# Performance work log

Measured on AMD Instinct MI355X. Metric: run time of the kernel, lower is better.

Reference implementation:

```python
import jax, jax.numpy as jnp
import numpy as np

N = 100000
E = 1600000
K = 3
DIMS = [64, 64, 64, 32, 16]


def setup_inputs() -> dict:
    key = jax.random.key(0)
    ks = jax.random.split(key, 12)
    inp = {
        "x": jax.random.normal(ks[0], (N, DIMS[0]), jnp.float32),
        "edge_index": jax.random.randint(ks[1], (2, E), 0, N, dtype=jnp.int64),
        "edge_weight": jax.random.uniform(ks[2], (E,), jnp.float32),
    }
    for i in range(4):
        scale = 1.0 / np.sqrt(DIMS[i] * K).astype(np.float32)
        inp[f"W{i+1}"] = jax.random.normal(ks[3 + 2 * i], (K, DIMS[i], DIMS[i + 1]), jnp.float32) * scale
        inp[f"b{i+1}"] = jnp.zeros((DIMS[i + 1],), jnp.float32)
    return inp


def _cheb_norm(edge_index, edge_weight, n):
    # PyG ChebConv norm with normalization='sym', lambda_max=2:
    # L = I - D^{-1/2} A D^{-1/2}; L_hat = 2L/lambda_max - I = -D^{-1/2} A D^{-1/2} (zero diag)
    row, col = edge_index[0], edge_index[1]
    w = jnp.where(row == col, 0.0, edge_weight)  # remove self loops
    deg = jax.ops.segment_sum(w, row, num_segments=n)
    dinv = jnp.where(deg > 0, jax.lax.rsqrt(deg), 0.0)  # inf -> 0 masking
    return -dinv[row] * w * dinv[col]


def _cheb_conv(x, edge_index, norm, W, b):
    row, col = edge_index[0], edge_index[1]
    n = x.shape[0]

    def prop(t):  # sparse L_hat @ t via gather + segment scatter-add
        return jax.ops.segment_sum(norm[:, None] * t[row], col, num_segments=n)

    Tx0 = x
    out = Tx0 @ W[0]
    Tx1 = prop(Tx0)
    out = out + Tx1 @ W[1]
    for k in range(2, W.shape[0]):
        Tx2 = 2.0 * prop(Tx1) - Tx0  # Chebyshev recurrence
        out = out + Tx2 @ W[k]
        Tx0, Tx1 = Tx1, Tx2
    return out + b


def reference(x, edge_index, edge_weight, W1, b1, W2, b2, W3, b3, W4, b4):
    norm = _cheb_norm(edge_index, edge_weight, x.shape[0])
    h = x
    for W, b in ((W1, b1), (W2, b2), (W3, b3), (W4, b4)):
        h = jax.nn.sigmoid(_cheb_conv(h, edge_index, norm, W, b))
    return h
```

## Files before the change

kernel.cpp:

```cpp
#include <hip/hip_runtime.h>
#include <math.h>


typedef __attribute__((ext_vector_type(8))) short short8_t;
typedef __attribute__((ext_vector_type(4))) short short4_t;
typedef __attribute__((ext_vector_type(4))) float f32x4;

#define NPP 512
#define FSH 9
#define CHUNK 2048
#define NXCD 8

__device__ __forceinline__ float bf2f(short s) {
    return __int_as_float(((int)(unsigned short)s) << 16);
}
__device__ __forceinline__ short f2bf(float f) {
    unsigned u = __float_as_uint(f);
    return (short)((u + 0x7FFFu + ((u >> 16) & 1u)) >> 16);
}

__device__ __forceinline__ int chunk_of_block(int bid, int B) {
    int xcd = bid & (NXCD - 1);
    int i = bid >> 3;
    int q = B >> 3, r = B & (NXCD - 1);
    return (xcd < r) ? xcd * (q + 1) + i : r * (q + 1) + (xcd - r) * q + i;
}

__device__ __forceinline__ int epk_row(unsigned u) { return (int)(u & 0x1FFFFu); }
__device__ __forceinline__ float epk_val(unsigned u) {
    return __uint_as_float((u >> 17) << 17);
}


__global__ __launch_bounds__(256) void f2b_kernel(
        const float* __restrict__ in, short* __restrict__ out, long m) {
    long i = ((long)blockIdx.x * 256 + threadIdx.x) * 4;
    if (i >= m) return;
    float4 v = *reinterpret_cast<const float4*>(in + i);
    short4_t s;
    s[0] = f2bf(v.x); s[1] = f2bf(v.y); s[2] = f2bf(v.z); s[3] = f2bf(v.w);
    *reinterpret_cast<short4_t*>(out + i) = s;
}


__global__ __launch_bounds__(256) void prep_kernel(
        const float* __restrict__ W1, const float* __restrict__ W2,
        const float* __restrict__ W3, const float* __restrict__ W4,
        short8_t* __restrict__ wpk1, short8_t* __restrict__ wpk2,
        short8_t* __restrict__ wpkm, short8_t* __restrict__ wpk4) {
    int idx = blockIdx.x * 256 + threadIdx.x;
    if (idx >= 4032) return;
    short8_t out;
    if (idx < 3072) {
        const float* W = (idx < 1536) ? W1 : W2;
        int f = (idx < 1536) ? idx : idx - 1536;
        int lane = f & 63, ct = (f >> 6) & 3, s = f >> 8;
        int li = lane & 15, lg = lane >> 4;
        int p = s >> 1;
        int col = ct * 16 + li;
#pragma unroll
        for (int e = 0; e < 8; ++e) {
            int k = (s & 1) * 32 + lg * 8 + e;
            int base = k * 64 + col;
            float v = (p == 0) ? W[base] - W[8192 + base]
                    : (p == 1) ? W[4096 + base]
                               : 2.0f * W[8192 + base];
            out[e] = f2bf(v);
        }
        ((idx < 1536) ? wpk1 : wpk2)[f] = out;
    } else if (idx < 3840) {
        int f = idx - 3072;
        int lane = f & 63, q = f >> 6;
        int s = q / 6, ct = q % 6;
        int li = lane & 15, lg = lane >> 4;
        int g = ct >> 1;
        int cl = (ct & 1) * 16 + li;
#pragma unroll
        for (int e = 0; e < 8; ++e) {
            int k = s * 32 + lg * 8 + e;
            int base = k * 32 + cl;
            float v = (g == 0) ? W3[base] - W3[4096 + base]
                    : (g == 1) ? W3[2048 + base]
                               : W3[4096 + base];
            out[e] = f2bf(v);
        }
        wpkm[f] = out;
    } else {
        int f = idx - 3840;
        int lane = f & 63, s = f >> 6;
        int li = lane & 15, lg = lane >> 4;
#pragma unroll
        for (int e = 0; e < 8; ++e) {
            int k = lg * 8 + e;
            int base = k * 16 + li;
            float v = (s == 0) ? W4[base] - W4[1024 + base]
                    : (s == 1) ? W4[512 + base]
                               : 2.0f * W4[1024 + base];
            out[e] = f2bf(v);
        }
        wpk4[f] = out;
    }
}


__global__ __launch_bounds__(256) void count_kernel(
        const int* __restrict__ row, const int* __restrict__ col,
        int* __restrict__ cntC, int* __restrict__ cntR, int P, int E) {
    __shared__ int hc[2][256], hr[2][256];
    for (int i = threadIdx.x; i < P; i += 256) {
        hc[0][i] = 0; hc[1][i] = 0; hr[0][i] = 0; hr[1][i] = 0;
    }
    __syncthreads();
    int chunk = chunk_of_block(blockIdx.x, gridDim.x);
    int cp = threadIdx.x & 1;
    int base = chunk * CHUNK;
    int lim = min(E, base + CHUNK);
    for (int e = base + threadIdx.x; e < lim; e += 256) {
        atomicAdd(&hc[cp][col[e] >> FSH], 1);
        atomicAdd(&hr[cp][row[e] >> FSH], 1);
    }
    __syncthreads();
    long o = (long)chunk * P;
    for (int i = threadIdx.x; i < P; i += 256) {
        cntC[o + i] = hc[0][i] + hc[1][i];
        cntR[o + i] = hr[0][i] + hr[1][i];
    }
}

__global__ __launch_bounds__(256) void colscan_kernel(
        int* __restrict__ cntC, int* __restrict__ cntR,
        int* __restrict__ ptotC, int* __restrict__ ptotR, int P, int B) {
    int bid = blockIdx.x;
    int* m; int* ptot; int p;
    if (bid < P) { m = cntC; ptot = ptotC; p = bid; }
    else         { m = cntR; ptot = ptotR; p = bid - P; }
    __shared__ int sh[256];
    int run = 0;
    for (int b0 = 0; b0 < B; b0 += 256) {
        int b = b0 + threadIdx.x;
        int v = (b < B) ? m[(long)b * P + p] : 0;
        sh[threadIdx.x] = v;
        __syncthreads();
        for (int o = 1; o < 256; o <<= 1) {
            int t = (threadIdx.x >= o) ? sh[threadIdx.x - o] : 0;
            __syncthreads();
            sh[threadIdx.x] += t;
            __syncthreads();
        }
        if (b < B) m[(long)b * P + p] = run + sh[threadIdx.x] - v;
        run += sh[255];
        __syncthreads();
    }
    if (threadIdx.x == 0) ptot[p] = run;
}

__global__ __launch_bounds__(256) void pscan_kernel(
        const int* __restrict__ ptotC, const int* __restrict__ ptotR,
        int* __restrict__ pofsC, int* __restrict__ pofsR,
        int* __restrict__ ofs, int P, int n, int E) {
    __shared__ int sh[256];
    int tid = threadIdx.x;
    int v = (tid < P) ? ptotC[tid] : 0;
    sh[tid] = v;
    __syncthreads();
    for (int o = 1; o < 256; o <<= 1) {
        int t = (tid >= o) ? sh[tid - o] : 0;
        __syncthreads();
        sh[tid] += t;
        __syncthreads();
    }
    if (tid < P) pofsC[tid] = sh[tid] - v;
    if (tid == 0) pofsC[P] = E;
    __syncthreads();
    v = (tid < P) ? ptotR[tid] : 0;
    sh[tid] = v;
    __syncthreads();
    for (int o = 1; o < 256; o <<= 1) {
        int t = (tid >= o) ? sh[tid - o] : 0;
        __syncthreads();
        sh[tid] += t;
        __syncthreads();
    }
    if (tid < P) pofsR[tid] = sh[tid] - v;
    if (tid == 0) { pofsR[P] = E; ofs[n] = E; }
}

__global__ __launch_bounds__(256) void scatter_kernel(
        const int* __restrict__ row, const int* __restrict__ col,
        const float* __restrict__ ew,
        const int* __restrict__ cntC, const int* __restrict__ cntR,
        const int* __restrict__ pofsC, const int* __restrict__ pofsR,
        int2* __restrict__ bufC, unsigned* __restrict__ bufR, int P, int E) {
    __shared__ int hc[256], hr[256];
    int chunk = chunk_of_block(blockIdx.x, gridDim.x);
    long o = (long)chunk * P;
    for (int i = threadIdx.x; i < P; i += 256) {
        hc[i] = pofsC[i] + cntC[o + i];
        hr[i] = pofsR[i] + cntR[o + i];
    }
    __syncthreads();
    int base = chunk * CHUNK;
    int lim = min(E, base + CHUNK);
    for (int e = base + threadIdx.x; e < lim; e += 256) {
        int r = row[e], c = col[e];
        float w = (r == c) ? 0.0f : ew[e];
        unsigned wb = __float_as_uint(w);
        int pc = atomicAdd(&hc[c >> FSH], 1);
        bufC[pc] = make_int2((int)(((unsigned)(c & (NPP - 1)) << 23) | (unsigned)r), (int)wb);
        int pr = atomicAdd(&hr[r >> FSH], 1);
        bufR[pr] = ((unsigned)(r & (NPP - 1)) << 23) | (wb >> 9);
    }
}

__global__ __launch_bounds__(512) void dinv_kernel(
        const unsigned* __restrict__ bufR, const int* __restrict__ rofs,
        float* __restrict__ dinv, int n) {
    int p = blockIdx.x;
    __shared__ float s[NPP];
    s[threadIdx.x] = 0.0f;
    __syncthreads();
    int beg = rofs[p], end = rofs[p + 1];
    for (int k = beg + threadIdx.x; k < end; k += 512) {
        unsigned u = bufR[k];
        atomicAdd(&s[u >> 23], __uint_as_float((u & 0x7FFFFFu) << 9));
    }
    __syncthreads();
    int node = (p << FSH) + threadIdx.x;
    if (node < n) {
        float d = s[threadIdx.x];
        dinv[node] = d > 0.0f ? rsqrtf(d) : 0.0f;
    }
}

__global__ __launch_bounds__(512) void fine_csr_kernel(
        const int2* __restrict__ bufC, const int* __restrict__ pofs,
        const float* __restrict__ dinv, int* __restrict__ ofs,
        unsigned* __restrict__ epk, int n) {
    int p = blockIdx.x;
    int tid = threadIdx.x;
    __shared__ int hist[NPP];
    __shared__ int sc[NPP];
    __shared__ float dc[NPP];
    hist[tid] = 0;
    int node = (p << FSH) + tid;
    dc[tid] = (node < n) ? dinv[node] : 0.0f;
    __syncthreads();
    int beg = pofs[p], end = pofs[p + 1];
    for (int k = beg + tid; k < end; k += 512)
        atomicAdd(&hist[((unsigned)bufC[k].x) >> 23], 1);
    __syncthreads();
    int v = hist[tid];
    sc[tid] = v;
    __syncthreads();
    for (int o = 1; o < 512; o <<= 1) {
        int t = (tid >= o) ? sc[tid - o] : 0;
        __syncthreads();
        sc[tid] += t;
        __syncthreads();
    }
    int mybase = beg + sc[tid] - v;
    if (node < n) ofs[node] = mybase;
    hist[tid] = mybase;
    __syncthreads();
    for (int k = beg + tid; k < end; k += 512) {
        int2 ed = bufC[k];
        unsigned key = (unsigned)ed.x;
        int fc = key >> 23;
        int r = (int)(key & 0x7FFFFFu);
        float w = __int_as_float(ed.y);
        float nrm = -dinv[r] * w * dc[fc];
        unsigned nb = __float_as_uint(nrm);
        unsigned n15 = (nb + 0xFFFFu + ((nb >> 17) & 1u)) >> 17;
        int pos = atomicAdd(&hist[fc], 1);
        epk[pos] = (n15 << 17) | (unsigned)r;
    }
}


template <int D>
__global__ __launch_bounds__(256) void agg_kernel(
        const int* __restrict__ ofs, const unsigned* __restrict__ epk,
        const short* __restrict__ tb, short* __restrict__ outb, int n) {
    constexpr int LPN = D / 8;
    int idx = blockIdx.x * 256 + threadIdx.x;
    int node = idx / LPN;
    int l = idx % LPN;
    if (node >= n) return;
    int beg = ofs[node], end = ofs[node + 1];
    float a[8] = {0.f, 0.f, 0.f, 0.f, 0.f, 0.f, 0.f, 0.f};
    const short* tc = tb + l * 8;
    int k = beg;
    for (; k + 8 <= end; k += 8) {
        unsigned ev[8];
        short8_t xv[8];
#pragma unroll
        for (int u = 0; u < 8; ++u) ev[u] = epk[k + u];
#pragma unroll
        for (int u = 0; u < 8; ++u)
            xv[u] = *reinterpret_cast<const short8_t*>(tc + (long)epk_row(ev[u]) * D);
#pragma unroll
        for (int u = 0; u < 8; ++u) {
            float v = epk_val(ev[u]);
#pragma unroll
            for (int j = 0; j < 8; ++j) a[j] = fmaf(v, bf2f(xv[u][j]), a[j]);
        }
    }
    for (; k + 4 <= end; k += 4) {
        unsigned ev[4];
        short8_t xv[4];
#pragma unroll
        for (int u = 0; u < 4; ++u) ev[u] = epk[k + u];
#pragma unroll
        for (int u = 0; u < 4; ++u)
            xv[u] = *reinterpret_cast<const short8_t*>(tc + (long)epk_row(ev[u]) * D);
#pragma unroll
        for (int u = 0; u < 4; ++u) {
            float v = epk_val(ev[u]);
#pragma unroll
            for (int j = 0; j < 8; ++j) a[j] = fmaf(v, bf2f(xv[u][j]), a[j]);
        }
    }
    for (; k < end; ++k) {
        unsigned e0 = epk[k];
        short8_t x0 = *reinterpret_cast<const short8_t*>(tc + (long)epk_row(e0) * D);
        float v = epk_val(e0);
#pragma unroll
        for (int j = 0; j < 8; ++j) a[j] = fmaf(v, bf2f(x0[j]), a[j]);
    }
    short8_t s;
#pragma unroll
    for (int j = 0; j < 8; ++j) s[j] = f2bf(a[j]);
    *reinterpret_cast<short8_t*>(outb + (long)node * D + l * 8) = s;
}


__global__ __launch_bounds__(256) void agg_dual_kernel(
        const int* __restrict__ ofs, const unsigned* __restrict__ epk,
        const short* __restrict__ tb, short* __restrict__ Q1b,
        short* __restrict__ Q2b, int n) {
    int idx = blockIdx.x * 256 + threadIdx.x;
    int node = idx >> 3;
    int l = idx & 7;
    if (node >= n) return;
    int beg = ofs[node], end = ofs[node + 1];
    float a[8] = {0.f, 0.f, 0.f, 0.f, 0.f, 0.f, 0.f, 0.f};
    const short* tc = tb + l * 8;
    int k = beg;
    for (; k + 8 <= end; k += 8) {
        unsigned ev[8];
        short8_t xv[8];
#pragma unroll
        for (int u = 0; u < 8; ++u) ev[u] = epk[k + u];
#pragma unroll
        for (int u = 0; u < 8; ++u)
            xv[u] = *reinterpret_cast<const short8_t*>(tc + (long)epk_row(ev[u]) * 64);
#pragma unroll
        for (int u = 0; u < 8; ++u) {
            float v = epk_val(ev[u]);
#pragma unroll
            for (int j = 0; j < 8; ++j) a[j] = fmaf(v, bf2f(xv[u][j]), a[j]);
        }
    }
    for (; k + 4 <= end; k += 4) {
        unsigned ev[4];
        short8_t xv[4];
#pragma unroll
        for (int u = 0; u < 4; ++u) ev[u] = epk[k + u];
#pragma unroll
        for (int u = 0; u < 4; ++u)
            xv[u] = *reinterpret_cast<const short8_t*>(tc + (long)epk_row(ev[u]) * 64);
#pragma unroll
        for (int u = 0; u < 4; ++u) {
            float v = epk_val(ev[u]);
#pragma unroll
            for (int j = 0; j < 8; ++j) a[j] = fmaf(v, bf2f(xv[u][j]), a[j]);
        }
    }
    for (; k < end; ++k) {
        unsigned e0 = epk[k];
        short8_t x0 = *reinterpret_cast<const short8_t*>(tc + (long)epk_row(e0) * 64);
        float v = epk_val(e0);
#pragma unroll
        for (int j = 0; j < 8; ++j) a[j] = fmaf(v, bf2f(x0[j]), a[j]);
    }
    short* ob = (l < 4) ? Q1b : Q2b;
    long o = (long)node * 32 + (l & 3) * 8;
    short8_t s;
#pragma unroll
    for (int j = 0; j < 8; ++j) s[j] = f2bf(a[j]);
    *reinterpret_cast<short8_t*>(ob + o) = s;
}


__global__ __launch_bounds__(256) void agg_fin_kernel(
        const int* __restrict__ ofs, const unsigned* __restrict__ epk,
        const short* __restrict__ Q2b, const float* __restrict__ S,
        const short* __restrict__ Q1b, short* __restrict__ outb, int n) {
    int idx = blockIdx.x * 256 + threadIdx.x;
    int node = idx >> 2;
    int l = idx & 3;
    if (node >= n) return;
    int beg = ofs[node], end = ofs[node + 1];
    float a[8] = {0.f, 0.f, 0.f, 0.f, 0.f, 0.f, 0.f, 0.f};
    const short* tc = Q2b + l * 8;
    int k = beg;
    for (; k + 4 <= end; k += 4) {
        unsigned ev[4];
        short8_t xv[4];
#pragma unroll
        for (int u = 0; u < 4; ++u) ev[u] = epk[k + u];
#pragma unroll
        for (int u = 0; u < 4; ++u)
            xv[u] = *reinterpret_cast<const short8_t*>(tc + (long)epk_row(ev[u]) * 32);
#pragma unroll
        for (int u = 0; u < 4; ++u) {
            float v = epk_val(ev[u]);
#pragma unroll
            for (int j = 0; j < 8; ++j) a[j] = fmaf(v, bf2f(xv[u][j]), a[j]);
        }
    }
    for (; k < end; ++k) {
        unsigned e0 = epk[k];
        short8_t x0 = *reinterpret_cast<const short8_t*>(tc + (long)epk_row(e0) * 32);
        float v = epk_val(e0);
#pragma unroll
        for (int j = 0; j < 8; ++j) a[j] = fmaf(v, bf2f(x0[j]), a[j]);
    }
    long o = (long)node * 32 + l * 8;
    float4 s0 = *reinterpret_cast<const float4*>(S + o);
    float4 s1 = *reinterpret_cast<const float4*>(S + o + 4);
    short8_t q1 = *reinterpret_cast<const short8_t*>(Q1b + o);
    float sv[8] = {s0.x, s0.y, s0.z, s0.w, s1.x, s1.y, s1.z, s1.w};
    short8_t r;
#pragma unroll
    for (int j = 0; j < 8; ++j) {
        float z = sv[j] + bf2f(q1[j]) + 2.0f * a[j];
        r[j] = f2bf(1.0f / (1.0f + expf(-z)));
    }
    *reinterpret_cast<short8_t*>(outb + o) = r;
}


__global__ __launch_bounds__(256) void gemm3_mfma(
        const short* __restrict__ t0b, const short* __restrict__ t1b,
        const short* __restrict__ t2b, const short8_t* __restrict__ wpk,
        const float* __restrict__ b, short* __restrict__ outb, int n) {
    const int tid = threadIdx.x;
    const int wave = tid >> 6;
    const int lane = tid & 63;
    const int li = lane & 15;
    const int lg = lane >> 4;

    short8_t bfr[6][4];
#pragma unroll
    for (int s = 0; s < 6; ++s)
#pragma unroll
        for (int ct = 0; ct < 4; ++ct)
            bfr[s][ct] = wpk[(s * 4 + ct) * 64 + lane];

    float bias_v[4];
#pragma unroll
    for (int ct = 0; ct < 4; ++ct) bias_v[ct] = b[ct * 16 + li];

#pragma unroll
    for (int t = 0; t < 2; ++t) {
        int r0 = blockIdx.x * 128 + wave * 32 + t * 16;
        if (r0 >= n) continue;
        int rA = r0 + li;
        if (rA >= n) rA = n - 1;
        f32x4 acc[4] = {{0.f, 0.f, 0.f, 0.f}, {0.f, 0.f, 0.f, 0.f},
                        {0.f, 0.f, 0.f, 0.f}, {0.f, 0.f, 0.f, 0.f}};
#pragma unroll
        for (int s = 0; s < 6; ++s) {
            const short* src = (s < 2) ? t0b : (s < 4) ? t1b : t2b;
            int k = (s & 1) * 32 + lg * 8;
            short8_t a = *reinterpret_cast<const short8_t*>(src + (long)rA * 64 + k);
#pragma unroll
            for (int ct = 0; ct < 4; ++ct)
                acc[ct] = __builtin_amdgcn_mfma_f32_16x16x32_bf16(a, bfr[s][ct], acc[ct], 0, 0, 0);
        }
#pragma unroll
        for (int ct = 0; ct < 4; ++ct) {
#pragma unroll
            for (int reg = 0; reg < 4; ++reg) {
                int row = r0 + lg * 4 + reg;
                if (row < n) {
                    float z = acc[ct][reg] + bias_v[ct];
                    float res = 1.0f / (1.0f + expf(-z));
                    outb[(long)row * 64 + ct * 16 + li] = f2bf(res);
                }
            }
        }
    }
}

__global__ __launch_bounds__(256) void gemm_multi_mfma(
        const short* __restrict__ hb, const short8_t* __restrict__ wpk,
        const float* __restrict__ b, short* __restrict__ P12b,
        float* __restrict__ S, int n) {
    const int tid = threadIdx.x;
    const int wave = tid >> 6;
    const int lane = tid & 63;
    const int li = lane & 15;
    const int lg = lane >> 4;

    short8_t bfr[2][6];
#pragma unroll
    for (int s = 0; s < 2; ++s)
#pragma unroll
        for (int ct = 0; ct < 6; ++ct)
            bfr[s][ct] = wpk[(s * 6 + ct) * 64 + lane];

    float bS0 = b[li], bS1 = b[16 + li];

#pragma unroll
    for (int t = 0; t < 2; ++t) {
        int r0 = blockIdx.x * 128 + wave * 32 + t * 16;
        if (r0 >= n) continue;
        int rA = r0 + li;
        if (rA >= n) rA = n - 1;
        f32x4 acc[6] = {{0.f, 0.f, 0.f, 0.f}, {0.f, 0.f, 0.f, 0.f},
                        {0.f, 0.f, 0.f, 0.f}, {0.f, 0.f, 0.f, 0.f},
                        {0.f, 0.f, 0.f, 0.f}, {0.f, 0.f, 0.f, 0.f}};
#pragma unroll
        for (int s = 0; s < 2; ++s) {
            int k = s * 32 + lg * 8;
            short8_t a = *reinterpret_cast<const short8_t*>(hb + (long)rA * 64 + k);
#pragma unroll
            for (int ct = 0; ct < 6; ++ct)
                acc[ct] = __builtin_amdgcn_mfma_f32_16x16x32_bf16(a, bfr[s][ct], acc[ct], 0, 0, 0);
        }
#pragma unroll
        for (int ct = 0; ct < 6; ++ct) {
            int g = ct >> 1;
            int cl = (ct & 1) * 16 + li;
#pragma unroll
            for (int reg = 0; reg < 4; ++reg) {
                int row = r0 + lg * 4 + reg;
                if (row >= n) continue;
                float v = acc[ct][reg];
                if (g == 0) {
                    S[(long)row * 32 + cl] = v + ((ct & 1) ? bS1 : bS0);
                } else if (g == 1) {
                    P12b[(long)row * 64 + cl] = f2bf(v);
                } else {
                    P12b[(long)row * 64 + 32 + cl] = f2bf(v);
                }
            }
        }
    }
}

__global__ __launch_bounds__(256) void gemm4_mfma(
        const short* __restrict__ t0b, const short* __restrict__ t1b,
        const short* __restrict__ t2b, const short8_t* __restrict__ wpk,
        const float* __restrict__ b, float* __restrict__ out, int n) {
    const int tid = threadIdx.x;
    const int wave = tid >> 6;
    const int lane = tid & 63;
    const int li = lane & 15;
    const int lg = lane >> 4;

    short8_t bfr[3];
#pragma unroll
    for (int s = 0; s < 3; ++s) bfr[s] = wpk[s * 64 + lane];

    float bias_v = b[li];

#pragma unroll
    for (int t = 0; t < 2; ++t) {
        int r0 = blockIdx.x * 128 + wave * 32 + t * 16;
        if (r0 >= n) continue;
        int rA = r0 + li;
        if (rA >= n) rA = n - 1;
        f32x4 acc = {0.f, 0.f, 0.f, 0.f};
        int k = lg * 8;
        short8_t a0 = *reinterpret_cast<const short8_t*>(t0b + (long)rA * 32 + k);
        acc = __builtin_amdgcn_mfma_f32_16x16x32_bf16(a0, bfr[0], acc, 0, 0, 0);
        short8_t a1 = *reinterpret_cast<const short8_t*>(t1b + (long)rA * 32 + k);
        acc = __builtin_amdgcn_mfma_f32_16x16x32_bf16(a1, bfr[1], acc, 0, 0, 0);
        short8_t a2 = *reinterpret_cast<const short8_t*>(t2b + (long)rA * 32 + k);
        acc = __builtin_amdgcn_mfma_f32_16x16x32_bf16(a2, bfr[2], acc, 0, 0, 0);
#pragma unroll
        for (int reg = 0; reg < 4; ++reg) {
            int row = r0 + lg * 4 + reg;
            if (row < n) {
                float z = acc[reg] + bias_v;
                out[(long)row * 16 + li] = 1.0f / (1.0f + expf(-z));
            }
        }
    }
}


static inline int ceil_div_l(long a, long b) { return (int)((a + b - 1) / b); }

extern "C" void kernel_launch(void* const* d_in, const int* in_sizes, int n_in,
                              void* d_out, int out_size, void* d_ws, size_t ws_size,
                              hipStream_t stream) {
    const float* x  = (const float*)d_in[0];
    const int*   ei = (const int*)d_in[1];
    const float* ew = (const float*)d_in[2];
    const float* W1 = (const float*)d_in[3];  const float* b1 = (const float*)d_in[4];
    const float* W2 = (const float*)d_in[5];  const float* b2 = (const float*)d_in[6];
    const float* W3 = (const float*)d_in[7];  const float* b3 = (const float*)d_in[8];
    const float* W4 = (const float*)d_in[9];  const float* b4 = (const float*)d_in[10];

    const int E = in_sizes[2];
    const int n = in_sizes[0] / 64;
    const int* row = ei;
    const int* col = ei + E;
    const int P = (n + NPP - 1) / NPP;
    const int B = (E + CHUNK - 1) / CHUNK;

    char* ws = (char*)d_ws;
    size_t off = 0;
    auto alloc = [&](size_t bytes) -> void* {
        void* p = ws + off;
        off += (bytes + 255) & ~(size_t)255;
        return p;
    };
    int*      cntC = (int*)alloc((size_t)B * P * sizeof(int));
    int*      cntR = (int*)alloc((size_t)B * P * sizeof(int));
    int*      ptotC = (int*)alloc(256 * sizeof(int));
    int*      ptotR = (int*)alloc(256 * sizeof(int));
    int*      pofsC = (int*)alloc((256 + 1) * sizeof(int));
    int*      pofsR = (int*)alloc((256 + 1) * sizeof(int));
    float*    dinv = (float*)alloc((size_t)n * sizeof(float));
    int*      ofs  = (int*)alloc((size_t)(n + 1) * sizeof(int));
    int2*     bufC = (int2*)alloc((size_t)E * sizeof(int2));
    unsigned* bufR = (unsigned*)alloc((size_t)E * sizeof(unsigned));
    unsigned* epk  = (unsigned*)alloc((size_t)E * sizeof(unsigned));
    short*    hbA  = (short*)alloc((size_t)n * 64 * sizeof(short));
    short*    hbB  = (short*)alloc((size_t)n * 64 * sizeof(short));
    short*    t1b  = (short*)alloc((size_t)n * 64 * sizeof(short));
    short*    Ub   = (short*)alloc((size_t)n * 64 * sizeof(short));
    float*    S    = (float*)alloc((size_t)n * 32 * sizeof(float));
    short8_t* wpk1 = (short8_t*)alloc(1536 * sizeof(short8_t));
    short8_t* wpk2 = (short8_t*)alloc(1536 * sizeof(short8_t));
    short8_t* wpkm = (short8_t*)alloc(768 * sizeof(short8_t));
    short8_t* wpk4 = (short8_t*)alloc(192 * sizeof(short8_t));
    if (off > ws_size) return;

    f2b_kernel<<<ceil_div_l((long)n * 16, 256), 256, 0, stream>>>(x, hbA, (long)n * 64);
    prep_kernel<<<16, 256, 0, stream>>>(W1, W2, W3, W4, wpk1, wpk2, wpkm, wpk4);

    count_kernel<<<B, 256, 0, stream>>>(row, col, cntC, cntR, P, E);
    colscan_kernel<<<2 * P, 256, 0, stream>>>(cntC, cntR, ptotC, ptotR, P, B);
    pscan_kernel<<<1, 256, 0, stream>>>(ptotC, ptotR, pofsC, pofsR, ofs, P, n, E);
    scatter_kernel<<<B, 256, 0, stream>>>(row, col, ew, cntC, cntR, pofsC, pofsR,
                                          bufC, bufR, P, E);
    dinv_kernel<<<P, 512, 0, stream>>>(bufR, pofsR, dinv, n);
    fine_csr_kernel<<<P, 512, 0, stream>>>(bufC, pofsC, dinv, ofs, epk, n);

    const int ab64 = ceil_div_l((long)n * 8, 256);
    const int ab32 = ceil_div_l((long)n * 4, 256);
    const int gb = ceil_div_l(n, 128);

    agg_kernel<64><<<ab64, 256, 0, stream>>>(ofs, epk, hbA, t1b, n);
    agg_kernel<64><<<ab64, 256, 0, stream>>>(ofs, epk, t1b, Ub, n);
    gemm3_mfma<<<gb, 256, 0, stream>>>(hbA, t1b, Ub, wpk1, b1, hbB, n);

    agg_kernel<64><<<ab64, 256, 0, stream>>>(ofs, epk, hbB, t1b, n);
    agg_kernel<64><<<ab64, 256, 0, stream>>>(ofs, epk, t1b, Ub, n);
    gemm3_mfma<<<gb, 256, 0, stream>>>(hbB, t1b, Ub, wpk2, b2, hbA, n);

    {
        short* P12b = t1b;
        short* Q1b  = Ub;
        short* Q2b  = Ub + (size_t)n * 32;
        short* hb3  = hbB;
        gemm_multi_mfma<<<gb, 256, 0, stream>>>(hbA, wpkm, b3, P12b, S, n);
        agg_dual_kernel<<<ab64, 256, 0, stream>>>(ofs, epk, P12b, Q1b, Q2b, n);
        agg_fin_kernel<<<ab32, 256, 0, stream>>>(ofs, epk, Q2b, S, Q1b, hb3, n);
    }

    agg_kernel<32><<<ab32, 256, 0, stream>>>(ofs, epk, hbB, t1b, n);
    agg_kernel<32><<<ab32, 256, 0, stream>>>(ofs, epk, t1b, Ub, n);
    gemm4_mfma<<<gb, 256, 0, stream>>>(hbB, t1b, Ub, wpk4, b4, (float*)d_out, n);
}
```

Baseline: 360.1 us.

## Double CSR partition size to 1024 nodes and fuse input-conversion with weight prep

Result: slower. 376.1 us (+4.5%).

```diff
diff --git a/kernel.cpp b/kernel.cpp
--- a/kernel.cpp
+++ b/kernel.cpp
@@ -6,8 +6,8 @@
 typedef __attribute__((ext_vector_type(4))) short short4_t;
 typedef __attribute__((ext_vector_type(4))) float f32x4;
 
-#define NPP 512
-#define FSH 9
+#define NPP 1024
+#define FSH 10
 #define CHUNK 2048
 #define NXCD 8
 
@@ -32,25 +32,23 @@
 }
 
 
-__global__ __launch_bounds__(256) void f2b_kernel(
-        const float* __restrict__ in, short* __restrict__ out, long m) {
-    long i = ((long)blockIdx.x * 256 + threadIdx.x) * 4;
-    if (i >= m) return;
-    float4 v = *reinterpret_cast<const float4*>(in + i);
-    short4_t s;
-    s[0] = f2bf(v.x); s[1] = f2bf(v.y); s[2] = f2bf(v.z); s[3] = f2bf(v.w);
-    *reinterpret_cast<short4_t*>(out + i) = s;
-}
-
-
-__global__ __launch_bounds__(256) void prep_kernel(
+__global__ __launch_bounds__(256) void init_kernel(
+        const float* __restrict__ in, short* __restrict__ out, long m,
         const float* __restrict__ W1, const float* __restrict__ W2,
         const float* __restrict__ W3, const float* __restrict__ W4,
         short8_t* __restrict__ wpk1, short8_t* __restrict__ wpk2,
         short8_t* __restrict__ wpkm, short8_t* __restrict__ wpk4) {
-    int idx = blockIdx.x * 256 + threadIdx.x;
+    long gi = (long)blockIdx.x * 256 + threadIdx.x;
+    long i4 = gi * 4;
+    if (i4 < m) {
+        float4 v = *reinterpret_cast<const float4*>(in + i4);
+        short4_t s;
+        s[0] = f2bf(v.x); s[1] = f2bf(v.y); s[2] = f2bf(v.z); s[3] = f2bf(v.w);
+        *reinterpret_cast<short4_t*>(out + i4) = s;
+    }
+    int idx = (int)gi;
     if (idx >= 4032) return;
-    short8_t out;
+    short8_t o;
     if (idx < 3072) {
         const float* W = (idx < 1536) ? W1 : W2;
         int f = (idx < 1536) ? idx : idx - 1536;
@@ -65,9 +63,9 @@
             float v = (p == 0) ? W[base] - W[8192 + base]
                     : (p == 1) ? W[4096 + base]
                                : 2.0f * W[8192 + base];
-            out[e] = f2bf(v);
-        }
-        ((idx < 1536) ? wpk1 : wpk2)[f] = out;
+            o[e] = f2bf(v);
+        }
+        ((idx < 1536) ? wpk1 : wpk2)[f] = o;
     } else if (idx < 3840) {
         int f = idx - 3072;
         int lane = f & 63, q = f >> 6;
@@ -82,9 +80,9 @@
             float v = (g == 0) ? W3[base] - W3[4096 + base]
                     : (g == 1) ? W3[2048 + base]
                                : W3[4096 + base];
-            out[e] = f2bf(v);
-        }
-        wpkm[f] = out;
+            o[e] = f2bf(v);
+        }
+        wpkm[f] = o;
     } else {
         int f = idx - 3840;
         int lane = f & 63, s = f >> 6;
@@ -96,9 +94,9 @@
             float v = (s == 0) ? W4[base] - W4[1024 + base]
                     : (s == 1) ? W4[512 + base]
                                : 2.0f * W4[1024 + base];
-            out[e] = f2bf(v);
-        }
-        wpk4[f] = out;
+            o[e] = f2bf(v);
+        }
+        wpk4[f] = o;
     }
 }
 
@@ -106,7 +104,7 @@
 __global__ __launch_bounds__(256) void count_kernel(
         const int* __restrict__ row, const int* __restrict__ col,
         int* __restrict__ cntC, int* __restrict__ cntR, int P, int E) {
-    __shared__ int hc[2][256], hr[2][256];
+    __shared__ int hc[2][128], hr[2][128];
     for (int i = threadIdx.x; i < P; i += 256) {
         hc[0][i] = 0; hc[1][i] = 0; hr[0][i] = 0; hr[1][i] = 0;
     }
@@ -185,13 +183,14 @@
     if (tid == 0) { pofsR[P] = E; ofs[n] = E; }
 }
 
+
 __global__ __launch_bounds__(256) void scatter_kernel(
         const int* __restrict__ row, const int* __restrict__ col,
         const float* __restrict__ ew,
         const int* __restrict__ cntC, const int* __restrict__ cntR,
         const int* __restrict__ pofsC, const int* __restrict__ pofsR,
         int2* __restrict__ bufC, unsigned* __restrict__ bufR, int P, int E) {
-    __shared__ int hc[256], hr[256];
+    __shared__ int hc[128], hr[128];
     int chunk = chunk_of_block(blockIdx.x, gridDim.x);
     long o = (long)chunk * P;
     for (int i = threadIdx.x; i < P; i += 256) {
@@ -206,13 +205,13 @@
         float w = (r == c) ? 0.0f : ew[e];
         unsigned wb = __float_as_uint(w);
         int pc = atomicAdd(&hc[c >> FSH], 1);
-        bufC[pc] = make_int2((int)(((unsigned)(c & (NPP - 1)) << 23) | (unsigned)r), (int)wb);
+        bufC[pc] = make_int2((int)(((unsigned)(c & (NPP - 1)) << 22) | (unsigned)r), (int)wb);
         int pr = atomicAdd(&hr[r >> FSH], 1);
-        bufR[pr] = ((unsigned)(r & (NPP - 1)) << 23) | (wb >> 9);
-    }
-}
-
-__global__ __launch_bounds__(512) void dinv_kernel(
+        bufR[pr] = ((unsigned)(r & (NPP - 1)) << 22) | (wb >> 10);
+    }
+}
+
+__global__ __launch_bounds__(1024) void dinv_kernel(
         const unsigned* __restrict__ bufR, const int* __restrict__ rofs,
         float* __restrict__ dinv, int n) {
     int p = blockIdx.x;
@@ -220,9 +219,9 @@
     s[threadIdx.x] = 0.0f;
     __syncthreads();
     int beg = rofs[p], end = rofs[p + 1];
-    for (int k = beg + threadIdx.x; k < end; k += 512) {
+    for (int k = beg + threadIdx.x; k < end; k += 1024) {
         unsigned u = bufR[k];
-        atomicAdd(&s[u >> 23], __uint_as_float((u & 0x7FFFFFu) << 9));
+        atomicAdd(&s[u >> 22], __uint_as_float((u & 0x3FFFFFu) << 10));
     }
     __syncthreads();
     int node = (p << FSH) + threadIdx.x;
@@ -232,7 +231,7 @@
     }
 }
 
-__global__ __launch_bounds__(512) void fine_csr_kernel(
+__global__ __launch_bounds__(1024) void fine_csr_kernel(
         const int2* __restrict__ bufC, const int* __restrict__ pofs,
         const float* __restrict__ dinv, int* __restrict__ ofs,
         unsigned* __restrict__ epk, int n) {
@@ -246,13 +245,13 @@
     dc[tid] = (node < n) ? dinv[node] : 0.0f;
     __syncthreads();
     int beg = pofs[p], end = pofs[p + 1];
-    for (int k = beg + tid; k < end; k += 512)
-        atomicAdd(&hist[((unsigned)bufC[k].x) >> 23], 1);
+    for (int k = beg + tid; k < end; k += 1024)
+        atomicAdd(&hist[((unsigned)bufC[k].x) >> 22], 1);
     __syncthreads();
     int v = hist[tid];
     sc[tid] = v;
     __syncthreads();
-    for (int o = 1; o < 512; o <<= 1) {
+    for (int o = 1; o < 1024; o <<= 1) {
         int t = (tid >= o) ? sc[tid - o] : 0;
         __syncthreads();
         sc[tid] += t;
@@ -262,11 +261,11 @@
     if (node < n) ofs[node] = mybase;
     hist[tid] = mybase;
     __syncthreads();
-    for (int k = beg + tid; k < end; k += 512) {
+    for (int k = beg + tid; k < end; k += 1024) {
         int2 ed = bufC[k];
         unsigned key = (unsigned)ed.x;
-        int fc = key >> 23;
-        int r = (int)(key & 0x7FFFFFu);
+        int fc = key >> 22;
+        int r = (int)(key & 0x3FFFFFu);
         float w = __int_as_float(ed.y);
         float nrm = -dinv[r] * w * dc[fc];
         unsigned nb = __float_as_uint(nrm);
@@ -622,10 +621,10 @@
     };
     int*      cntC = (int*)alloc((size_t)B * P * sizeof(int));
     int*      cntR = (int*)alloc((size_t)B * P * sizeof(int));
-    int*      ptotC = (int*)alloc(256 * sizeof(int));
-    int*      ptotR = (int*)alloc(256 * sizeof(int));
-    int*      pofsC = (int*)alloc((256 + 1) * sizeof(int));
-    int*      pofsR = (int*)alloc((256 + 1) * sizeof(int));
+    int*      ptotC = (int*)alloc(128 * sizeof(int));
+    int*      ptotR = (int*)alloc(128 * sizeof(int));
+    int*      pofsC = (int*)alloc((128 + 1) * sizeof(int));
+    int*      pofsR = (int*)alloc((128 + 1) * sizeof(int));
     float*    dinv = (float*)alloc((size_t)n * sizeof(float));
     int*      ofs  = (int*)alloc((size_t)(n + 1) * sizeof(int));
     int2*     bufC = (int2*)alloc((size_t)E * sizeof(int2));
@@ -642,16 +641,16 @@
     short8_t* wpk4 = (short8_t*)alloc(192 * sizeof(short8_t));
     if (off > ws_size) return;
 
-    f2b_kernel<<<ceil_div_l((long)n * 16, 256), 256, 0, stream>>>(x, hbA, (long)n * 64);
-    prep_kernel<<<16, 256, 0, stream>>>(W1, W2, W3, W4, wpk1, wpk2, wpkm, wpk4);
+    init_kernel<<<ceil_div_l((long)n * 16, 256), 256, 0, stream>>>(
+        x, hbA, (long)n * 64, W1, W2, W3, W4, wpk1, wpk2, wpkm, wpk4);
 
     count_kernel<<<B, 256, 0, stream>>>(row, col, cntC, cntR, P, E);
     colscan_kernel<<<2 * P, 256, 0, stream>>>(cntC, cntR, ptotC, ptotR, P, B);
     pscan_kernel<<<1, 256, 0, stream>>>(ptotC, ptotR, pofsC, pofsR, ofs, P, n, E);
     scatter_kernel<<<B, 256, 0, stream>>>(row, col, ew, cntC, cntR, pofsC, pofsR,
                                           bufC, bufR, P, E);
-    dinv_kernel<<<P, 512, 0, stream>>>(bufR, pofsR, dinv, n);
-    fine_csr_kernel<<<P, 512, 0, stream>>>(bufC, pofsC, dinv, ofs, epk, n);
+    dinv_kernel<<<P, 1024, 0, stream>>>(bufR, pofsR, dinv, n);
+    fine_csr_kernel<<<P, 1024, 0, stream>>>(bufC, pofsC, dinv, ofs, epk, n);
 
     const int ab64 = ceil_div_l((long)n * 8, 256);
     const int ab32 = ceil_div_l((long)n * 4, 256);
```

## Merge x-to-bf16 and weight packing kernels; double edge chunk size

Applied to the files above, without the earlier changes.

Result: no change. 354.0 us (-1.7%).

```diff
diff --git a/kernel.cpp b/kernel.cpp
--- a/kernel.cpp
+++ b/kernel.cpp
@@ -8,7 +8,7 @@
 
 #define NPP 512
 #define FSH 9
-#define CHUNK 2048
+#define CHUNK 4096
 #define NXCD 8
 
 __device__ __forceinline__ float bf2f(short s) {
@@ -32,25 +32,23 @@
 }
 
 
-__global__ __launch_bounds__(256) void f2b_kernel(
-        const float* __restrict__ in, short* __restrict__ out, long m) {
-    long i = ((long)blockIdx.x * 256 + threadIdx.x) * 4;
-    if (i >= m) return;
-    float4 v = *reinterpret_cast<const float4*>(in + i);
-    short4_t s;
-    s[0] = f2bf(v.x); s[1] = f2bf(v.y); s[2] = f2bf(v.z); s[3] = f2bf(v.w);
-    *reinterpret_cast<short4_t*>(out + i) = s;
-}
-
-
-__global__ __launch_bounds__(256) void prep_kernel(
+__global__ __launch_bounds__(256) void init_kernel(
+        const float* __restrict__ in, short* __restrict__ out, long m,
         const float* __restrict__ W1, const float* __restrict__ W2,
         const float* __restrict__ W3, const float* __restrict__ W4,
         short8_t* __restrict__ wpk1, short8_t* __restrict__ wpk2,
         short8_t* __restrict__ wpkm, short8_t* __restrict__ wpk4) {
-    int idx = blockIdx.x * 256 + threadIdx.x;
+    long gi = (long)blockIdx.x * 256 + threadIdx.x;
+    long i4 = gi * 4;
+    if (i4 < m) {
+        float4 v = *reinterpret_cast<const float4*>(in + i4);
+        short4_t s;
+        s[0] = f2bf(v.x); s[1] = f2bf(v.y); s[2] = f2bf(v.z); s[3] = f2bf(v.w);
+        *reinterpret_cast<short4_t*>(out + i4) = s;
+    }
+    int idx = (int)gi;
     if (idx >= 4032) return;
-    short8_t out;
+    short8_t o;
     if (idx < 3072) {
         const float* W = (idx < 1536) ? W1 : W2;
         int f = (idx < 1536) ? idx : idx - 1536;
@@ -65,9 +63,9 @@
             float v = (p == 0) ? W[base] - W[8192 + base]
                     : (p == 1) ? W[4096 + base]
                                : 2.0f * W[8192 + base];
-            out[e] = f2bf(v);
-        }
-        ((idx < 1536) ? wpk1 : wpk2)[f] = out;
+            o[e] = f2bf(v);
+        }
+        ((idx < 1536) ? wpk1 : wpk2)[f] = o;
     } else if (idx < 3840) {
         int f = idx - 3072;
         int lane = f & 63, q = f >> 6;
@@ -82,9 +80,9 @@
             float v = (g == 0) ? W3[base] - W3[4096 + base]
                     : (g == 1) ? W3[2048 + base]
                                : W3[4096 + base];
-            out[e] = f2bf(v);
-        }
-        wpkm[f] = out;
+            o[e] = f2bf(v);
+        }
+        wpkm[f] = o;
     } else {
         int f = idx - 3840;
         int lane = f & 63, s = f >> 6;
@@ -96,9 +94,9 @@
             float v = (s == 0) ? W4[base] - W4[1024 + base]
                     : (s == 1) ? W4[512 + base]
                                : 2.0f * W4[1024 + base];
-            out[e] = f2bf(v);
-        }
-        wpk4[f] = out;
+            o[e] = f2bf(v);
+        }
+        wpk4[f] = o;
     }
 }
 
@@ -184,6 +182,7 @@
     if (tid < P) pofsR[tid] = sh[tid] - v;
     if (tid == 0) { pofsR[P] = E; ofs[n] = E; }
 }
+
 
 __global__ __launch_bounds__(256) void scatter_kernel(
         const int* __restrict__ row, const int* __restrict__ col,
@@ -642,8 +641,8 @@
     short8_t* wpk4 = (short8_t*)alloc(192 * sizeof(short8_t));
     if (off > ws_size) return;
 
-    f2b_kernel<<<ceil_div_l((long)n * 16, 256), 256, 0, stream>>>(x, hbA, (long)n * 64);
-    prep_kernel<<<16, 256, 0, stream>>>(W1, W2, W3, W4, wpk1, wpk2, wpkm, wpk4);
+    init_kernel<<<ceil_div_l((long)n * 16, 256), 256, 0, stream>>>(
+        x, hbA, (long)n * 64, W1, W2, W3, W4, wpk1, wpk2, wpkm, wpk4);
 
     count_kernel<<<B, 256, 0, stream>>>(row, col, cntC, cntR, P, E);
     colscan_kernel<<<2 * P, 256, 0, stream>>>(cntC, cntR, ptotC, ptotR, P, B);
```
